# Optimization experiments

Measured on AMD Instinct MI355X. Metric: run time of the kernel, lower is better.

## Reference

```python
import jax, jax.numpy as jnp
import numpy as np

N, D, DFF, H, L = 98280, 192, 384, 8, 36
S = N // L  # 2730 sets per partition
HD = D // H
EPS = 1e-5


def _ln(x, g, b):
    m = x.mean(-1, keepdims=True)
    v = ((x - m) ** 2).mean(-1, keepdims=True)
    return (x - m) * jax.lax.rsqrt(v + EPS) * g + b


def _mha(q, k, v, Wqkv, bqkv, Wo, bo, mask):
    # q,k,v: (S, L, D); mask: (S, L), True = padded key
    Wq, Wk, Wv = jnp.split(Wqkv, 3, axis=0)
    bq, bk, bv = jnp.split(bqkv, 3)
    qh = (q @ Wq.T + bq).reshape(S, L, H, HD)
    kh = (k @ Wk.T + bk).reshape(S, L, H, HD)
    vh = (v @ Wv.T + bv).reshape(S, L, H, HD)
    scores = jnp.einsum('slhd,smhd->shlm', qh, kh) / np.sqrt(HD).astype(np.float32)
    scores = jnp.where(mask[:, None, None, :], -1e9, scores)
    attn = jax.nn.softmax(scores, axis=-1)
    out = jnp.einsum('shlm,smhd->slhd', attn, vh).reshape(S, L, D)
    return out @ Wo.T + bo


def _layer(x, pos, inds, mask, Wqkv, bqkv, Wo, bo, W1, b1, W2, b2,
           g1, be1, g2, be2, gn, bn):
    identity = x
    sf = x[inds]                 # gather voxels into sets: (S, L, D)
    qk = sf + pos[inds]          # pos added to q and k only (value = sf)
    src2 = _mha(qk, qk, sf, Wqkv, bqkv, Wo, bo, mask)
    flat = inds.reshape(-1)
    # torch.unique(return_inverse) + flip + scatter == take FIRST occurrence
    # of each voxel id; .at[].min is deterministic under duplicates.
    perm = jnp.full((N,), flat.shape[0], jnp.int32).at[flat].min(
        jnp.arange(flat.shape[0], dtype=jnp.int32))
    src2 = src2.reshape(-1, D)[perm]   # scatter back: (N, D)
    x = _ln(x + src2, g1, be1)
    ff = jnp.maximum(x @ W1.T + b1, 0.0) @ W2.T + b2
    x = _ln(x + ff, g2, be2)
    return _ln(x + identity, gn, bn)   # DSVT_EncoderLayer residual norm


def reference(src, inds0, inds1, mask0, mask1, pos0, pos1,
              Wqkv, bqkv, Wo, bo, W1, b1, W2, b2,
              g1, be1, g2, be2, gn, bn, block_id):
    inds = (inds0, inds1)
    masks = (mask0, mask1)
    pos = (pos0, pos1)
    out = src
    for i in range(2):  # two set partitions within the shift (shift_id = block_id % 2)
        out = _layer(out, pos[i], inds[i], masks[i],
                     Wqkv[i], bqkv[i], Wo[i], bo[i],
                     W1[i], b1[i], W2[i], b2[i],
                     g1[i], be1[i], g2[i], be2[i], gn[i], bn[i])
    return out


def setup_inputs():
    key = jax.random.key(0)
    ks = jax.random.split(key, 16)
    sd = 0.02
    return {
        "src": jax.random.normal(ks[0], (N, D), jnp.float32),
        "inds0": jax.random.permutation(ks[1], N).reshape(S, L).astype(jnp.int32),
        "inds1": jax.random.permutation(ks[2], N).reshape(S, L).astype(jnp.int32),
        "mask0": jnp.zeros((S, L), bool),
        "mask1": jnp.zeros((S, L), bool),
        "pos0": jax.random.normal(ks[3], (N, D), jnp.float32),
        "pos1": jax.random.normal(ks[4], (N, D), jnp.float32),
        "Wqkv": sd * jax.random.normal(ks[5], (2, 3 * D, D), jnp.float32),
        "bqkv": jnp.zeros((2, 3 * D), jnp.float32),
        "Wo": sd * jax.random.normal(ks[6], (2, D, D), jnp.float32),
        "bo": jnp.zeros((2, D), jnp.float32),
        "W1": sd * jax.random.normal(ks[7], (2, DFF, D), jnp.float32),
        "b1": jnp.zeros((2, DFF), jnp.float32),
        "W2": sd * jax.random.normal(ks[8], (2, D, DFF), jnp.float32),
        "b2": jnp.zeros((2, D), jnp.float32),
        "g1": jnp.ones((2, D), jnp.float32),
        "be1": jnp.zeros((2, D), jnp.float32),
        "g2": jnp.ones((2, D), jnp.float32),
        "be2": jnp.zeros((2, D), jnp.float32),
        "gn": jnp.ones((2, D), jnp.float32),
        "bn": jnp.zeros((2, D), jnp.float32),
        "block_id": 0,
    }
```

## Files before the change

kernel.cpp:

```cpp
#include <hip/hip_runtime.h>
#include <stdint.h>

#define NVOX   98280
#define S_SETS 2730
#define L_SET  36
#define D_MODEL 192
#define D_FF    384
#define N_HEADS 8
#define H_DIM   24
#define CFP    200

using s16x8 = __attribute__((ext_vector_type(8))) short;
using s16x4 = __attribute__((ext_vector_type(4))) short;
using f32x4 = __attribute__((ext_vector_type(4))) float;

__device__ __forceinline__ float bf2f(unsigned short h) {
    unsigned u = ((unsigned)h) << 16;
    return __builtin_bit_cast(float, u);
}
__device__ __forceinline__ unsigned short f2bf(float f) {
    unsigned u = __builtin_bit_cast(unsigned, f);
    u += 0x7FFF + ((u >> 16) & 1);
    return (unsigned short)(u >> 16);
}

__global__ __launch_bounds__(256)
void convert_f32_bf16(const float* __restrict__ src, short* __restrict__ dst, int n)
{
    int i = blockIdx.x * 256 + threadIdx.x;
    if (i < n) dst[i] = (short)f2bf(src[i]);
}

__global__ __launch_bounds__(256)
void gather_kernel(const float* __restrict__ x, const float* __restrict__ pos,
                   const int* __restrict__ inds,
                   short* __restrict__ qk, short* __restrict__ sf)
{
    int f = blockIdx.x * 4 + (threadIdx.x >> 6);
    int lane = threadIdx.x & 63;
    if (lane >= 48) return;
    int v = inds[f];
    float4 a = *(const float4*)(x + (size_t)v * D_MODEL + lane * 4);
    float4 p = *(const float4*)(pos + (size_t)v * D_MODEL + lane * 4);
    s16x4 q, s;
    q[0] = (short)f2bf(a.x + p.x); q[1] = (short)f2bf(a.y + p.y);
    q[2] = (short)f2bf(a.z + p.z); q[3] = (short)f2bf(a.w + p.w);
    s[0] = (short)f2bf(a.x); s[1] = (short)f2bf(a.y);
    s[2] = (short)f2bf(a.z); s[3] = (short)f2bf(a.w);
    *(s16x4*)(qk + (size_t)f * D_MODEL + lane * 4) = q;
    *(s16x4*)(sf + (size_t)f * D_MODEL + lane * 4) = s;
}

__global__ __launch_bounds__(512, 4)
void qkv_direct(const short* __restrict__ qk, const short* __restrict__ sf,
                const short* __restrict__ W, const float* __restrict__ bias,
                short* __restrict__ C, int n)
{
    __shared__ char Bs[36864];
    const int bx = blockIdx.x;
    const int sec = bx >> 1, half = bx & 1;
    const int colOff = sec * 192 + half * 96;
    const short* Ap = (sec == 2) ? sf : qk;
    const short* Wp = W + (size_t)colOff * 192;
    const int rowBase = blockIdx.y * 128;
    const int tid = threadIdx.x;

    #pragma unroll
    for (int t = tid; t < 2304; t += 512) {
        int row = t / 24, c8 = t % 24;
        s16x8 v = *(const s16x8*)(Wp + (size_t)row * 192 + c8 * 8);
        *(s16x8*)(Bs + row * 384 + ((c8 * 16) ^ ((row & 7) << 4))) = v;
    }
    __syncthreads();

    const int wid = tid >> 6, lane = tid & 63;
    const int lr = lane & 15, kb = lane >> 4;
    const int arow = rowBase + wid * 16 + lr;
    const bool rv = arow < n;
    const short* Arow = Ap + (size_t)arow * 192 + kb * 8;

    f32x4 acc[6] = {};
    #pragma unroll
    for (int ks = 0; ks < 6; ++ks) {
        s16x8 a = {};
        if (rv) a = *(const s16x8*)(Arow + ks * 32);
        s16x8 b[6];
        #pragma unroll
        for (int fj = 0; fj < 6; ++fj) {
            int row = fj * 16 + lr;
            b[fj] = *(const s16x8*)(Bs + row * 384 + ((ks * 64 + kb * 16) ^ ((row & 7) << 4)));
        }
        #pragma unroll
        for (int fj = 0; fj < 6; ++fj)
            acc[fj] = __builtin_amdgcn_mfma_f32_16x16x32_bf16(a, b[fj], acc[fj], 0, 0, 0);
    }
    #pragma unroll
    for (int fj = 0; fj < 6; ++fj) {
        int col = colOff + fj * 16 + lr;
        float bv = bias[col];
        #pragma unroll
        for (int r = 0; r < 4; ++r) {
            int grow = rowBase + wid * 16 + kb * 4 + r;
            if (grow < n)
                C[(size_t)grow * 576 + col] = (short)f2bf(acc[fj][r] + bv);
        }
    }
}

__global__ __launch_bounds__(256)
void attn_mfma(const short* __restrict__ qkv, const unsigned char* __restrict__ mask,
               short* __restrict__ attn_out)
{
    __shared__ short Plall[4 * 48 * 64];
    const int wid = threadIdx.x >> 6;
    const int lane = threadIdx.x & 63;
    const int p = blockIdx.x * 4 + wid;
    const int s = p >> 3;
    const int h = p & 7;
    short* Pl = Plall + wid * 48 * 64;
    char* Pb = (char*)Pl;
    const int lr = lane & 15, g = lane >> 4;

    #pragma unroll
    for (int i = 0; i < 6; ++i)
        *(s16x8*)(Pl + i * 512 + lane * 8) = (s16x8){};

    s16x8 qa[3], kb3[3];
    #pragma unroll
    for (int t = 0; t < 3; ++t) {
        int rr = t * 16 + lr;
        qa[t] = (s16x8){};
        kb3[t] = (s16x8){};
        if (rr < L_SET && g < 3) {
            const short* base = qkv + (size_t)(s * L_SET + rr) * 576 + h * H_DIM + g * 8;
            qa[t] = *(const s16x8*)(base);
            kb3[t] = *(const s16x8*)(base + 192);
        }
    }
    f32x4 sc[3][3] = {};
    #pragma unroll
    for (int mt = 0; mt < 3; ++mt)
        #pragma unroll
        for (int nt = 0; nt < 3; ++nt)
            sc[mt][nt] = __builtin_amdgcn_mfma_f32_16x16x32_bf16(qa[mt], kb3[nt], sc[mt][nt], 0, 0, 0);

    s16x8 vb[2][2];
    #pragma unroll
    for (int ks = 0; ks < 2; ++ks)
        #pragma unroll
        for (int nt = 0; nt < 2; ++nt)
            #pragma unroll
            for (int e = 0; e < 8; ++e) {
                size_t row = (size_t)s * L_SET + ks * 32 + g * 8 + e;
                vb[ks][nt][e] = qkv[row * 576 + 384 + h * H_DIM + nt * 16 + lr];
            }

    const float scale = 0.20412414523193154f;
    bool colmask[3];
    #pragma unroll
    for (int nt = 0; nt < 3; ++nt) {
        int m = nt * 16 + lr;
        colmask[nt] = (m >= L_SET) || (mask[(size_t)s * L_SET + (m < L_SET ? m : 0)] != 0);
    }
    #pragma unroll
    for (int mt = 0; mt < 3; ++mt) {
        #pragma unroll
        for (int r = 0; r < 4; ++r) {
            float v[3], ev[3];
            #pragma unroll
            for (int nt = 0; nt < 3; ++nt)
                v[nt] = colmask[nt] ? -1e9f : sc[mt][nt][r] * scale;
            float mx = fmaxf(fmaxf(v[0], v[1]), v[2]);
            #pragma unroll
            for (int off = 1; off < 16; off <<= 1) mx = fmaxf(mx, __shfl_xor(mx, off, 64));
            float sm = 0.f;
            #pragma unroll
            for (int nt = 0; nt < 3; ++nt) { ev[nt] = __expf(v[nt] - mx); sm += ev[nt]; }
            #pragma unroll
            for (int off = 1; off < 16; off <<= 1) sm += __shfl_xor(sm, off, 64);
            float rinv = 1.f / sm;
            int q = mt * 16 + g * 4 + r;
            #pragma unroll
            for (int nt = 0; nt < 3; ++nt) {
                int m = nt * 16 + lr;
                *(short*)(Pb + q * 128 + ((m * 2) ^ ((q & 7) << 4))) =
                    (short)f2bf(ev[nt] * rinv);
            }
        }
    }

    f32x4 o[3][2] = {};
    #pragma unroll
    for (int ks = 0; ks < 2; ++ks) {
        s16x8 pa[3];
        #pragma unroll
        for (int mt = 0; mt < 3; ++mt) {
            int row = mt * 16 + lr;
            pa[mt] = *(const s16x8*)(Pb + row * 128 + ((ks * 64 + g * 16) ^ ((row & 7) << 4)));
        }
        #pragma unroll
        for (int mt = 0; mt < 3; ++mt)
            #pragma unroll
            for (int nt = 0; nt < 2; ++nt)
                o[mt][nt] = __builtin_amdgcn_mfma_f32_16x16x32_bf16(pa[mt], vb[ks][nt], o[mt][nt], 0, 0, 0);
    }

    #pragma unroll
    for (int mt = 0; mt < 3; ++mt) {
        #pragma unroll
        for (int nt = 0; nt < 2; ++nt) {
            #pragma unroll
            for (int r = 0; r < 4; ++r) {
                int q = mt * 16 + g * 4 + r;
                int d = nt * 16 + lr;
                if (q < L_SET && d < H_DIM)
                    attn_out[(size_t)(s * L_SET + q) * D_MODEL + h * H_DIM + d] =
                        (short)f2bf(o[mt][nt][r]);
            }
        }
    }
}

__device__ __forceinline__ float wave_sum64(float v) {
    #pragma unroll
    for (int off = 32; off > 0; off >>= 1) v += __shfl_xor(v, off, 64);
    return v;
}

__global__ __launch_bounds__(512)
void wo_ln1(const short* __restrict__ attnb, const short* __restrict__ Wo,
            const float* __restrict__ bo, const int* __restrict__ inds,
            const float* __restrict__ xin,
            const float* __restrict__ g1, const float* __restrict__ be1,
            short* __restrict__ x1, int n)
{
    extern __shared__ char pool[];
    char* As = pool;
    char* Bs = pool + 49152;
    float* Cf = (float*)pool;
    const int rowBase = blockIdx.x * 128;
    const int tid = threadIdx.x;
    const int wid = tid >> 6, lane = tid & 63;
    const int lr = lane & 15, kb = lane >> 4;
    const int wm = wid & 3, wn = wid >> 2;

    int vv[16];
    #pragma unroll
    for (int i = 0; i < 16; ++i) {
        int f = rowBase + wid * 16 + i;
        vv[i] = (f < n) ? inds[f] : 0;
    }
    float4 gv = (lane < 48) ? *(const float4*)(g1 + lane * 4) : make_float4(0,0,0,0);
    float4 bv = (lane < 48) ? *(const float4*)(be1 + lane * 4) : make_float4(0,0,0,0);

    #pragma unroll
    for (int t = tid; t < 3072; t += 512) {
        int row = t / 24, c8 = t % 24;
        int grow = rowBase + row;
        s16x8 v = {};
        if (grow < n) v = *(const s16x8*)(attnb + (size_t)grow * 192 + c8 * 8);
        *(s16x8*)(As + row * 384 + ((c8 * 16) ^ ((row & 7) << 4))) = v;
    }
    #pragma unroll
    for (int t = tid; t < 4608; t += 512) {
        int row = t / 24, c8 = t % 24;
        s16x8 v = *(const s16x8*)(Wo + (size_t)row * 192 + c8 * 8);
        *(s16x8*)(Bs + row * 384 + ((c8 * 16) ^ ((row & 7) << 4))) = v;
    }
    __syncthreads();

    float4 xr[16];
    #pragma unroll
    for (int i = 0; i < 16; ++i)
        xr[i] = (lane < 48) ? *(const float4*)(xin + (size_t)vv[i] * D_MODEL + lane * 4)
                            : make_float4(0.f, 0.f, 0.f, 0.f);

    f32x4 acc[2][6] = {};
    #pragma unroll
    for (int ks = 0; ks < 6; ++ks) {
        s16x8 a[2], b[6];
        #pragma unroll
        for (int fi = 0; fi < 2; ++fi) {
            int row = wm * 32 + fi * 16 + lr;
            a[fi] = *(const s16x8*)(As + row * 384 + ((ks * 64 + kb * 16) ^ ((row & 7) << 4)));
        }
        #pragma unroll
        for (int fj = 0; fj < 6; ++fj) {
            int row = wn * 96 + fj * 16 + lr;
            b[fj] = *(const s16x8*)(Bs + row * 384 + ((ks * 64 + kb * 16) ^ ((row & 7) << 4)));
        }
        #pragma unroll
        for (int fi = 0; fi < 2; ++fi)
            #pragma unroll
            for (int fj = 0; fj < 6; ++fj)
                acc[fi][fj] = __builtin_amdgcn_mfma_f32_16x16x32_bf16(a[fi], b[fj], acc[fi][fj], 0, 0, 0);
    }
    __syncthreads();
    #pragma unroll
    for (int fj = 0; fj < 6; ++fj) {
        int col = wn * 96 + fj * 16 + lr;
        float bvv = bo[col];
        #pragma unroll
        for (int fi = 0; fi < 2; ++fi)
            #pragma unroll
            for (int r = 0; r < 4; ++r) {
                int row = wm * 32 + fi * 16 + kb * 4 + r;
                Cf[row * CFP + col] = acc[fi][fj][r] + bvv;
            }
    }
    __syncthreads();

    #pragma unroll
    for (int i = 0; i < 16; ++i) {
        int r = wid * 16 + i;
        int f = rowBase + r;
        float4 t = make_float4(0.f, 0.f, 0.f, 0.f);
        if (lane < 48) {
            float4 c4 = *(const float4*)&Cf[r * CFP + lane * 4];
            t.x = c4.x + xr[i].x; t.y = c4.y + xr[i].y;
            t.z = c4.z + xr[i].z; t.w = c4.w + xr[i].w;
        }
        float mean = wave_sum64(t.x + t.y + t.z + t.w) * (1.f / 192.f);
        float ss   = wave_sum64(t.x*t.x + t.y*t.y + t.z*t.z + t.w*t.w) * (1.f / 192.f);
        float inv = rsqrtf(ss - mean * mean + 1e-5f);
        if (lane < 48 && f < n) {
            s16x4 o;
            o[0] = (short)f2bf((t.x - mean) * inv * gv.x + bv.x);
            o[1] = (short)f2bf((t.y - mean) * inv * gv.y + bv.y);
            o[2] = (short)f2bf((t.z - mean) * inv * gv.z + bv.z);
            o[3] = (short)f2bf((t.w - mean) * inv * gv.w + bv.w);
            *(s16x4*)(x1 + (size_t)vv[i] * D_MODEL + lane * 4) = o;
        }
    }
}

__global__ __launch_bounds__(512)
void ffn_fused(const short* __restrict__ x1, const short* __restrict__ W1,
               const float* __restrict__ b1, const short* __restrict__ W2,
               const float* __restrict__ b2, const float* __restrict__ xin,
               const float* __restrict__ g2, const float* __restrict__ be2,
               const float* __restrict__ gn, const float* __restrict__ bn,
               float* __restrict__ outp, int n)
{
    extern __shared__ char pool[];
    char* Ax  = pool;
    char* W1c = pool + 49152;
    char* W2c = pool + 86016;
    char* Hc  = pool + 125952;
    float* Cf = (float*)(pool + 49152);
    const int rowBase = blockIdx.x * 128;
    const int tid = threadIdx.x;
    const int wid = tid >> 6, lane = tid & 63;
    const int lr = lane & 15, kb = lane >> 4;
    const int wm = wid & 3, wn = wid >> 2;

    s16x8 w1r[5], w2r[5];
    #pragma unroll
    for (int i = 0; i < 5; ++i) {
        int t = i * 512 + tid;
        w1r[i] = (s16x8){}; w2r[i] = (s16x8){};
        if (t < 2304) {
            int row = t / 24, c8 = t % 24;
            w1r[i] = *(const s16x8*)(W1 + (size_t)row * 192 + c8 * 8);
            int row2 = t / 12, c82 = t % 12;
            w2r[i] = *(const s16x8*)(W2 + (size_t)row2 * 384 + c82 * 8);
        }
    }

    #pragma unroll
    for (int t = tid; t < 3072; t += 512) {
        int row = t / 24, c8 = t % 24;
        int grow = rowBase + row;
        s16x8 v = {};
        if (grow < n) v = *(const s16x8*)(x1 + (size_t)grow * 192 + c8 * 8);
        *(s16x8*)(Ax + row * 384 + ((c8 * 16) ^ ((row & 7) << 4))) = v;
    }

    f32x4 acc2[2][6] = {};
    for (int c = 0; c < 4; ++c) {
        __syncthreads();
        #pragma unroll
        for (int i = 0; i < 5; ++i) {
            int t = i * 512 + tid;
            if (t < 2304) {
                int row = t / 24, c8 = t % 24;
                *(s16x8*)(W1c + row * 384 + ((c8 * 16) ^ ((row & 7) << 4))) = w1r[i];
                int row2 = t / 12, c82 = t % 12;
                *(s16x8*)(W2c + row2 * 208 + c82 * 16) = w2r[i];
            }
        }
        __syncthreads();
        if (c < 3) {
            #pragma unroll
            for (int i = 0; i < 5; ++i) {
                int t = i * 512 + tid;
                if (t < 2304) {
                    int row = t / 24, c8 = t % 24;
                    w1r[i] = *(const s16x8*)(W1 + (size_t)((c + 1) * 96 + row) * 192 + c8 * 8);
                    int row2 = t / 12, c82 = t % 12;
                    w2r[i] = *(const s16x8*)(W2 + (size_t)row2 * 384 + (c + 1) * 96 + c82 * 8);
                }
            }
        }
        f32x4 acc1[2][3] = {};
        #pragma unroll
        for (int ks = 0; ks < 6; ++ks) {
            s16x8 a[2], b[3];
            #pragma unroll
            for (int fi = 0; fi < 2; ++fi) {
                int row = wm * 32 + fi * 16 + lr;
                a[fi] = *(const s16x8*)(Ax + row * 384 + ((ks * 64 + kb * 16) ^ ((row & 7) << 4)));
            }
            #pragma unroll
            for (int fj = 0; fj < 3; ++fj) {
                int row = wn * 48 + fj * 16 + lr;
                b[fj] = *(const s16x8*)(W1c + row * 384 + ((ks * 64 + kb * 16) ^ ((row & 7) << 4)));
            }
            #pragma unroll
            for (int fi = 0; fi < 2; ++fi)
                #pragma unroll
                for (int fj = 0; fj < 3; ++fj)
                    acc1[fi][fj] = __builtin_amdgcn_mfma_f32_16x16x32_bf16(a[fi], b[fj], acc1[fi][fj], 0, 0, 0);
        }
        #pragma unroll
        for (int fj = 0; fj < 3; ++fj) {
            int col = wn * 48 + fj * 16 + lr;
            float b1v = b1[c * 96 + col];
            #pragma unroll
            for (int fi = 0; fi < 2; ++fi)
                #pragma unroll
                for (int r = 0; r < 4; ++r) {
                    int row = wm * 32 + fi * 16 + kb * 4 + r;
                    *(short*)(Hc + row * 208 + col * 2) =
                        (short)f2bf(fmaxf(acc1[fi][fj][r] + b1v, 0.f));
                }
        }
        __syncthreads();
        #pragma unroll
        for (int ks = 0; ks < 3; ++ks) {
            s16x8 a[2], b[6];
            #pragma unroll
            for (int fi = 0; fi < 2; ++fi) {
                int row = wm * 32 + fi * 16 + lr;
                a[fi] = *(const s16x8*)(Hc + row * 208 + ks * 64 + kb * 16);
            }
            #pragma unroll
            for (int fj = 0; fj < 6; ++fj) {
                int row = wn * 96 + fj * 16 + lr;
                b[fj] = *(const s16x8*)(W2c + row * 208 + ks * 64 + kb * 16);
            }
            #pragma unroll
            for (int fi = 0; fi < 2; ++fi)
                #pragma unroll
                for (int fj = 0; fj < 6; ++fj)
                    acc2[fi][fj] = __builtin_amdgcn_mfma_f32_16x16x32_bf16(a[fi], b[fj], acc2[fi][fj], 0, 0, 0);
        }
    }

    float4 xr[16];
    #pragma unroll
    for (int i = 0; i < 16; ++i) {
        int gvx = rowBase + wid * 16 + i;
        xr[i] = (lane < 48 && gvx < n)
              ? *(const float4*)(xin + (size_t)gvx * D_MODEL + lane * 4)
              : make_float4(0.f, 0.f, 0.f, 0.f);
    }
    float4 g2v = (lane < 48) ? *(const float4*)(g2 + lane * 4) : make_float4(0,0,0,0);
    float4 b2v = (lane < 48) ? *(const float4*)(be2 + lane * 4) : make_float4(0,0,0,0);
    float4 gnv = (lane < 48) ? *(const float4*)(gn + lane * 4) : make_float4(0,0,0,0);
    float4 bnv = (lane < 48) ? *(const float4*)(bn + lane * 4) : make_float4(0,0,0,0);

    __syncthreads();
    #pragma unroll
    for (int fj = 0; fj < 6; ++fj) {
        int col = wn * 96 + fj * 16 + lr;
        float bvv = b2[col];
        #pragma unroll
        for (int fi = 0; fi < 2; ++fi)
            #pragma unroll
            for (int r = 0; r < 4; ++r) {
                int row = wm * 32 + fi * 16 + kb * 4 + r;
                Cf[row * CFP + col] = acc2[fi][fj][r] + bvv;
            }
    }
    __syncthreads();

    #pragma unroll
    for (int i = 0; i < 16; ++i) {
        int r = wid * 16 + i;
        int gvx = rowBase + r;
        float4 t = make_float4(0.f, 0.f, 0.f, 0.f);
        if (lane < 48) {
            float4 f4 = *(const float4*)&Cf[r * CFP + lane * 4];
            int byteoff = r * 384 + (((lane >> 1) << 4) ^ ((r & 7) << 4)) + ((lane & 1) << 3);
            s16x4 xv = *(const s16x4*)(Ax + byteoff);
            t.x = f4.x + bf2f((unsigned short)xv[0]);
            t.y = f4.y + bf2f((unsigned short)xv[1]);
            t.z = f4.z + bf2f((unsigned short)xv[2]);
            t.w = f4.w + bf2f((unsigned short)xv[3]);
        }
        float m1 = wave_sum64(t.x + t.y + t.z + t.w) * (1.f / 192.f);
        float s1 = wave_sum64(t.x*t.x + t.y*t.y + t.z*t.z + t.w*t.w) * (1.f / 192.f);
        float i1 = rsqrtf(s1 - m1 * m1 + 1e-5f);
        float4 t2 = make_float4(0.f, 0.f, 0.f, 0.f);
        if (lane < 48) {
            t2.x = (t.x - m1) * i1 * g2v.x + b2v.x + xr[i].x;
            t2.y = (t.y - m1) * i1 * g2v.y + b2v.y + xr[i].y;
            t2.z = (t.z - m1) * i1 * g2v.z + b2v.z + xr[i].z;
            t2.w = (t.w - m1) * i1 * g2v.w + b2v.w + xr[i].w;
        }
        float m2 = wave_sum64(t2.x + t2.y + t2.z + t2.w) * (1.f / 192.f);
        float s2 = wave_sum64(t2.x*t2.x + t2.y*t2.y + t2.z*t2.z + t2.w*t2.w) * (1.f / 192.f);
        float i2 = rsqrtf(s2 - m2 * m2 + 1e-5f);
        if (lane < 48 && gvx < n) {
            float4 o;
            o.x = (t2.x - m2) * i2 * gnv.x + bnv.x;
            o.y = (t2.y - m2) * i2 * gnv.y + bnv.y;
            o.z = (t2.z - m2) * i2 * gnv.z + bnv.z;
            o.w = (t2.w - m2) * i2 * gnv.w + bnv.w;
            *(float4*)(outp + (size_t)gvx * D_MODEL + lane * 4) = o;
        }
    }
}

extern "C" void kernel_launch(void* const* d_in, const int* in_sizes, int n_in,
                              void* d_out, int out_size, void* d_ws, size_t ws_size,
                              hipStream_t stream)
{
    (void)in_sizes; (void)n_in; (void)out_size;
    const int N = NVOX;
    const float* src = (const float*)d_in[0];
    const int* inds[2] = {(const int*)d_in[1], (const int*)d_in[2]};
    const unsigned char* mask[2] = {(const unsigned char*)d_in[3], (const unsigned char*)d_in[4]};
    const float* pos[2] = {(const float*)d_in[5], (const float*)d_in[6]};
    const float* Wqkv = (const float*)d_in[7];
    const float* bqkv = (const float*)d_in[8];
    const float* Wo   = (const float*)d_in[9];
    const float* bo   = (const float*)d_in[10];
    const float* W1   = (const float*)d_in[11];
    const float* b1   = (const float*)d_in[12];
    const float* W2   = (const float*)d_in[13];
    const float* b2   = (const float*)d_in[14];
    const float* g1   = (const float*)d_in[15];
    const float* be1  = (const float*)d_in[16];
    const float* g2   = (const float*)d_in[17];
    const float* be2  = (const float*)d_in[18];
    const float* gn   = (const float*)d_in[19];
    const float* bn   = (const float*)d_in[20];

    float* out = (float*)d_out;
    short* wsS = (short*)d_ws;

    const size_t NE = (size_t)N * D_MODEL;
    short* wqkv_b = wsS;
    short* wo_b   = wsS + 221184;
    short* w1_b   = wsS + 294912;
    short* w2_b   = wsS + 442368;
    const size_t base = 1048576;
    short* qk    = wsS + base;
    short* sf    = qk + NE;
    short* qkvb  = sf + NE;
    short* attnb = qkvb + 3 * NE;
    short* x1    = attnb + NE;

    if (ws_size < (base + 7 * NE) * sizeof(short)) return;

    const dim3 blk(256);
    convert_f32_bf16<<<dim3(864), blk, 0, stream>>>(Wqkv, wqkv_b, 221184);
    convert_f32_bf16<<<dim3(288), blk, 0, stream>>>(Wo,   wo_b,   73728);
    convert_f32_bf16<<<dim3(576), blk, 0, stream>>>(W1,   w1_b,   147456);
    convert_f32_bf16<<<dim3(576), blk, 0, stream>>>(W2,   w2_b,   147456);

    const int RT = (N + 127) / 128;
    for (int i = 0; i < 2; ++i) {
        const float* xin = (i == 0) ? src : out;
        gather_kernel<<<dim3(24570), blk, 0, stream>>>(xin, pos[i], inds[i], qk, sf);
        qkv_direct<<<dim3(6, RT), dim3(512), 0, stream>>>(
            qk, sf, wqkv_b + (size_t)i * 110592, bqkv + i * 576, qkvb, N);
        attn_mfma<<<dim3(S_SETS * N_HEADS / 4), dim3(256), 0, stream>>>(qkvb, mask[i], attnb);
        wo_ln1<<<dim3(RT), dim3(512), 122880, stream>>>(
            attnb, wo_b + (size_t)i * 36864, bo + i * 192, inds[i], xin,
            g1 + i * 192, be1 + i * 192, x1, N);
        ffn_fused<<<dim3(RT), dim3(512), 152576, stream>>>(
            x1, w1_b + (size_t)i * 73728, b1 + i * 384, w2_b + (size_t)i * 73728,
            b2 + i * 192, xin, g2 + i * 192, be2 + i * 192,
            gn + i * 192, bn + i * 192, out, N);
    }
}
```

Before: 688.4 us.

## Double ffn_fused block to 1024 threads with one M-fragment per wave

Raises the fused FFN kernel from 512 to 1024 threads per block and remaps the 128-row tile onto 16 waves (8 along M, 2 along N). Each wave now handles a single 16-row fragment, so the MFMA accumulators, weight prefetch registers and per-wave row loop all shrink. The aim is more waves per CU to hide LDS and global latency, since the 152 KB of shared memory limits residency to one block per CU. The cost is that B fragments are re-read from LDS by twice as many waves, and barriers now synchronize more waves.

```diff
diff --git a/kernel.cpp b/kernel.cpp
--- a/kernel.cpp
+++ b/kernel.cpp
@@ -334,7 +334,7 @@
     }
 }
 
-__global__ __launch_bounds__(512)
+__global__ __launch_bounds__(1024)
 void ffn_fused(const short* __restrict__ x1, const short* __restrict__ W1,
                const float* __restrict__ b1, const short* __restrict__ W2,
                const float* __restrict__ b2, const float* __restrict__ xin,
@@ -352,12 +352,13 @@
     const int tid = threadIdx.x;
     const int wid = tid >> 6, lane = tid & 63;
     const int lr = lane & 15, kb = lane >> 4;
-    const int wm = wid & 3, wn = wid >> 2;
-
-    s16x8 w1r[5], w2r[5];
-    #pragma unroll
-    for (int i = 0; i < 5; ++i) {
-        int t = i * 512 + tid;
+    const int wm = wid & 7;
+    const int wn = wid >> 3;
+
+    s16x8 w1r[3], w2r[3];
+    #pragma unroll
+    for (int i = 0; i < 3; ++i) {
+        int t = i * 1024 + tid;
         w1r[i] = (s16x8){}; w2r[i] = (s16x8){};
         if (t < 2304) {
             int row = t / 24, c8 = t % 24;
@@ -368,7 +369,7 @@
     }
 
     #pragma unroll
-    for (int t = tid; t < 3072; t += 512) {
+    for (int t = tid; t < 3072; t += 1024) {
         int row = t / 24, c8 = t % 24;
         int grow = rowBase + row;
         s16x8 v = {};
@@ -376,12 +377,12 @@
         *(s16x8*)(Ax + row * 384 + ((c8 * 16) ^ ((row & 7) << 4))) = v;
     }
 
-    f32x4 acc2[2][6] = {};
+    f32x4 acc2[6] = {};
     for (int c = 0; c < 4; ++c) {
         __syncthreads();
         #pragma unroll
-        for (int i = 0; i < 5; ++i) {
-            int t = i * 512 + tid;
+        for (int i = 0; i < 3; ++i) {
+            int t = i * 1024 + tid;
             if (t < 2304) {
                 int row = t / 24, c8 = t % 24;
                 *(s16x8*)(W1c + row * 384 + ((c8 * 16) ^ ((row & 7) << 4))) = w1r[i];
@@ -392,8 +393,8 @@
         __syncthreads();
         if (c < 3) {
             #pragma unroll
-            for (int i = 0; i < 5; ++i) {
-                int t = i * 512 + tid;
+            for (int i = 0; i < 3; ++i) {
+                int t = i * 1024 + tid;
                 if (t < 2304) {
                     int row = t / 24, c8 = t % 24;
                     w1r[i] = *(const s16x8*)(W1 + (size_t)((c + 1) * 96 + row) * 192 + c8 * 8);
@@ -402,65 +403,53 @@
                 }
             }
         }
-        f32x4 acc1[2][3] = {};
+        f32x4 acc1[3] = {};
         #pragma unroll
         for (int ks = 0; ks < 6; ++ks) {
-            s16x8 a[2], b[3];
-            #pragma unroll
-            for (int fi = 0; fi < 2; ++fi) {
-                int row = wm * 32 + fi * 16 + lr;
-                a[fi] = *(const s16x8*)(Ax + row * 384 + ((ks * 64 + kb * 16) ^ ((row & 7) << 4)));
-            }
+            int row = wm * 16 + lr;
+            s16x8 a = *(const s16x8*)(Ax + row * 384 + ((ks * 64 + kb * 16) ^ ((row & 7) << 4)));
+            s16x8 b[3];
             #pragma unroll
             for (int fj = 0; fj < 3; ++fj) {
-                int row = wn * 48 + fj * 16 + lr;
-                b[fj] = *(const s16x8*)(W1c + row * 384 + ((ks * 64 + kb * 16) ^ ((row & 7) << 4)));
-            }
-            #pragma unroll
-            for (int fi = 0; fi < 2; ++fi)
-                #pragma unroll
-                for (int fj = 0; fj < 3; ++fj)
-                    acc1[fi][fj] = __builtin_amdgcn_mfma_f32_16x16x32_bf16(a[fi], b[fj], acc1[fi][fj], 0, 0, 0);
+                int brow = wn * 48 + fj * 16 + lr;
+                b[fj] = *(const s16x8*)(W1c + brow * 384 + ((ks * 64 + kb * 16) ^ ((brow & 7) << 4)));
+            }
+            #pragma unroll
+            for (int fj = 0; fj < 3; ++fj)
+                acc1[fj] = __builtin_amdgcn_mfma_f32_16x16x32_bf16(a, b[fj], acc1[fj], 0, 0, 0);
         }
         #pragma unroll
         for (int fj = 0; fj < 3; ++fj) {
             int col = wn * 48 + fj * 16 + lr;
             float b1v = b1[c * 96 + col];
             #pragma unroll
-            for (int fi = 0; fi < 2; ++fi)
-                #pragma unroll
-                for (int r = 0; r < 4; ++r) {
-                    int row = wm * 32 + fi * 16 + kb * 4 + r;
-                    *(short*)(Hc + row * 208 + col * 2) =
-                        (short)f2bf(fmaxf(acc1[fi][fj][r] + b1v, 0.f));
-                }
+            for (int r = 0; r < 4; ++r) {
+                int row = wm * 16 + kb * 4 + r;
+                *(short*)(Hc + row * 208 + col * 2) =
+                    (short)f2bf(fmaxf(acc1[fj][r] + b1v, 0.f));
+            }
         }
         __syncthreads();
         #pragma unroll
         for (int ks = 0; ks < 3; ++ks) {
-            s16x8 a[2], b[6];
-            #pragma unroll
-            for (int fi = 0; fi < 2; ++fi) {
-                int row = wm * 32 + fi * 16 + lr;
-                a[fi] = *(const s16x8*)(Hc + row * 208 + ks * 64 + kb * 16);
-            }
+            int row = wm * 16 + lr;
+            s16x8 a = *(const s16x8*)(Hc + row * 208 + ks * 64 + kb * 16);
+            s16x8 b[6];
             #pragma unroll
             for (int fj = 0; fj < 6; ++fj) {
-                int row = wn * 96 + fj * 16 + lr;
-                b[fj] = *(const s16x8*)(W2c + row * 208 + ks * 64 + kb * 16);
-            }
-            #pragma unroll
-            for (int fi = 0; fi < 2; ++fi)
-                #pragma unroll
-                for (int fj = 0; fj < 6; ++fj)
-                    acc2[fi][fj] = __builtin_amdgcn_mfma_f32_16x16x32_bf16(a[fi], b[fj], acc2[fi][fj], 0, 0, 0);
-        }
-    }
-
-    float4 xr[16];
-    #pragma unroll
-    for (int i = 0; i < 16; ++i) {
-        int gvx = rowBase + wid * 16 + i;
+                int brow = wn * 96 + fj * 16 + lr;
+                b[fj] = *(const s16x8*)(W2c + brow * 208 + ks * 64 + kb * 16);
+            }
+            #pragma unroll
+            for (int fj = 0; fj < 6; ++fj)
+                acc2[fj] = __builtin_amdgcn_mfma_f32_16x16x32_bf16(a, b[fj], acc2[fj], 0, 0, 0);
+        }
+    }
+
+    float4 xr[8];
+    #pragma unroll
+    for (int i = 0; i < 8; ++i) {
+        int gvx = rowBase + wid * 8 + i;
         xr[i] = (lane < 48 && gvx < n)
               ? *(const float4*)(xin + (size_t)gvx * D_MODEL + lane * 4)
               : make_float4(0.f, 0.f, 0.f, 0.f);
@@ -476,18 +465,16 @@
         int col = wn * 96 + fj * 16 + lr;
         float bvv = b2[col];
         #pragma unroll
-        for (int fi = 0; fi < 2; ++fi)
-            #pragma unroll
-            for (int r = 0; r < 4; ++r) {
-                int row = wm * 32 + fi * 16 + kb * 4 + r;
-                Cf[row * CFP + col] = acc2[fi][fj][r] + bvv;
-            }
+        for (int r = 0; r < 4; ++r) {
+            int row = wm * 16 + kb * 4 + r;
+            Cf[row * CFP + col] = acc2[fj][r] + bvv;
+        }
     }
     __syncthreads();
 
     #pragma unroll
-    for (int i = 0; i < 16; ++i) {
-        int r = wid * 16 + i;
+    for (int i = 0; i < 8; ++i) {
+        int r = wid * 8 + i;
         int gvx = rowBase + r;
         float4 t = make_float4(0.f, 0.f, 0.f, 0.f);
         if (lane < 48) {
@@ -581,7 +568,7 @@
         wo_ln1<<<dim3(RT), dim3(512), 122880, stream>>>(
             attnb, wo_b + (size_t)i * 36864, bo + i * 192, inds[i], xin,
             g1 + i * 192, be1 + i * 192, x1, N);
-        ffn_fused<<<dim3(RT), dim3(512), 152576, stream>>>(
+        ffn_fused<<<dim3(RT), dim3(1024), 152576, stream>>>(
             x1, w1_b + (size_t)i * 73728, b1 + i * 384, w2_b + (size_t)i * 73728,
             b2 + i * 192, xin, g2 + i * 192, be2 + i * 192,
             gn + i * 192, bn + i * 192, out, N);
```

Measured after the change: 678.5 us. About the same (-1.4%).
